# Performance work log

Measured on AMD Instinct MI355X. Metric: run time of the kernel, lower is better.

The kernel has to match this reference:

```python
import jax, jax.numpy as jnp
import numpy as np

PAD = 1
STRIDE = (1, 1)
TEMPERATURE = 1.0


def setup_inputs() -> dict:
    key = jax.random.key(0)
    ks = jax.random.split(key, 5)
    x = jax.random.normal(ks[0], (16, 256, 56, 56), dtype=jnp.float32)
    kernels = jax.random.normal(ks[1], (8, 256, 256, 3, 3), dtype=jnp.float32)
    w1 = jax.random.normal(ks[2], (256, 64), dtype=jnp.float32) * 0.0625
    b1 = jnp.zeros((64,), dtype=jnp.float32)
    w2 = jax.random.normal(ks[3], (64, 8), dtype=jnp.float32) * 0.125
    b2 = jnp.zeros((8,), dtype=jnp.float32)
    return {"x": x, "kernels": kernels, "w1": w1, "b1": b1, "w2": w2, "b2": b2}


def _forward(x, kernels, w1, b1, w2, b2):
    # Attention: global average pool -> MLP -> softmax over kernels
    pooled = jnp.mean(x, axis=(2, 3))                      # [B, C]
    h = jax.nn.relu(pooled @ w1 + b1)                      # [B, H]
    scores = h @ w2 + b2                                   # [B, K]
    alphas = jax.nn.softmax(scores / TEMPERATURE, axis=-1) # [B, K]

    # Per-sample mixed kernels: [B, O, I, kh, kw]
    weighted = jnp.einsum('bk,koihw->boihw', alphas, kernels)

    # Per-sample conv2d (groups=1), vectorized over batch
    def conv_one(xi, wi):
        return jax.lax.conv_general_dilated(
            xi[None], wi, STRIDE, [(PAD, PAD), (PAD, PAD)],
            dimension_numbers=('NCHW', 'OIHW', 'NCHW'))[0]

    return jax.vmap(conv_one)(x, weighted)                 # [B, O, H, W]


def reference(x, kernels, w1, b1, w2, b2):
    return _forward(x, kernels, w1, b1, w2, b2)
```

## Files before the change

### kernel.cpp

```cpp
#include <hip/hip_runtime.h>
#include <hip/hip_bf16.h>
#include <stdint.h>

typedef __attribute__((ext_vector_type(8))) short bf16x8;
typedef __attribute__((ext_vector_type(4))) float f32x4;

#define BATCH 16
#define CH    256
#define HW    56
#define HWHW  3136
#define NK    8

#define XPT_BYTES   30408704ul
#define WK_BYTES    18874368ul
#define POOL_BYTES  16384ul
#define ALPHA_BYTES 512ul

__device__ __forceinline__ void gl_lds16(const void* g, void* l) {
    __builtin_amdgcn_global_load_lds((const __attribute__((address_space(1))) uint32_t*)g,
                                     (__attribute__((address_space(3))) uint32_t*)l, 16, 0, 0);
}

__device__ __forceinline__ float bf16bits_to_f32(short h) {
    return __uint_as_float(((uint32_t)(uint16_t)h) << 16);
}

__global__ void __launch_bounds__(256, 2)
xpose_pool_kernel(const float* __restrict__ x, __hip_bfloat16* __restrict__ xp,
                  float* __restrict__ pooled) {
    __shared__ short tile[2 * 56 * 256];
    const int tid = threadIdx.x;
    const int ys  = blockIdx.x;
    const int b   = blockIdx.y;
    const int y0  = ys * 2;

    const float* xb = x + (size_t)b * CH * HWHW + (size_t)y0 * HW;
    for (int it = 0; it < 28; ++it) {
        int idx = it * 256 + tid;
        int ch  = idx / 28;
        int xi  = idx - ch * 28;
        int r   = xi / 14;
        int x4  = (xi - r * 14) * 4;
        const float4 v = *(const float4*)(xb + (size_t)ch * HWHW + r * HW + x4);
        const float* vf = (const float*)&v;
#pragma unroll
        for (int j = 0; j < 4; ++j) {
            __hip_bfloat16 h = __float2bfloat16(vf[j]);
            tile[(r * 56 + x4 + j) * 256 + (ch ^ (((x4 & 7) | j) << 3))] = *(const short*)&h;
        }
    }
    __syncthreads();

    {
        float s = 0.f;
        const int ch = tid;
        for (int r = 0; r < 2; ++r)
            for (int xx = 0; xx < 56; ++xx)
                s += bf16bits_to_f32(tile[(r * 56 + xx) * 256 + (ch ^ ((xx & 7) << 3))]);
        atomicAdd(&pooled[b * 256 + ch], s * (1.0f / 3136.0f));
    }

    __hip_bfloat16* dst0 = xp + ((size_t)(b * 58 + y0 + 1) * 64 + 1) * 256;
    for (int it = 0; it < 14; ++it) {
        int idx = it * 256 + tid;
        int ch0 = (idx & 31) * 8;
        int pos = idx >> 5;
        int r = pos / 56, xx = pos - (pos / 56) * 56;
        bf16x8 vv = *(const bf16x8*)&tile[(r * 56 + xx) * 256 + (ch0 ^ ((xx & 7) << 3))];
        *(bf16x8*)(dst0 + ((size_t)(r * 64 + xx)) * 256 + ch0) = vv;
    }

    bf16x8 z = {};
    if (tid < 128) {
        int r   = tid >> 6;
        int c2  = (tid >> 5) & 1;
        int ch0 = (tid & 31) * 8;
        *(bf16x8*)(xp + ((size_t)(b * 58 + y0 + 1 + r) * 64 + (c2 ? 57 : 0)) * 256 + ch0) = z;
    }
    if (ys == 0 || ys == 27) {
        int p = (ys == 0) ? 0 : 57;
        __hip_bfloat16* rowp = xp + (size_t)(b * 58 + p) * 64 * 256;
        for (int it = tid; it < 2048; it += 256)
            *(bf16x8*)(rowp + (size_t)it * 8) = z;
    }
}

__global__ void __launch_bounds__(256)
mlp_kernel(const float* __restrict__ pooled,
           const float* __restrict__ w1, const float* __restrict__ b1,
           const float* __restrict__ w2, const float* __restrict__ b2,
           float* __restrict__ alphas) {
    const int b = blockIdx.x;
    __shared__ float pl[256];
    __shared__ float hp[4][64];
    __shared__ float h[64];
    __shared__ float sc[8];
    int t = threadIdx.x;
    pl[t] = pooled[b * 256 + t];
    __syncthreads();
    int j = t & 63, part = t >> 6;
    float s = 0.f;
    const float* w1p = w1 + part * 64 * 64 + j;
#pragma unroll 8
    for (int c = 0; c < 64; ++c) s += pl[part * 64 + c] * w1p[c * 64];
    hp[part][j] = s;
    __syncthreads();
    if (t < 64) h[t] = fmaxf(hp[0][t] + hp[1][t] + hp[2][t] + hp[3][t] + b1[t], 0.f);
    __syncthreads();
    if (t < 8) {
        float acc = b2[t];
#pragma unroll 8
        for (int jj = 0; jj < 64; ++jj) acc += h[jj] * w2[jj * 8 + t];
        sc[t] = acc;
    }
    __syncthreads();
    if (t == 0) {
        float m = sc[0];
#pragma unroll
        for (int k = 1; k < 8; ++k) m = fmaxf(m, sc[k]);
        float ssum = 0.f, e[8];
#pragma unroll
        for (int k = 0; k < 8; ++k) { e[k] = expf(sc[k] - m); ssum += e[k]; }
        float inv = 1.0f / ssum;
#pragma unroll
        for (int k = 0; k < 8; ++k) alphas[b * 8 + k] = e[k] * inv;
    }
}

__global__ void wmix_kernel(const float* __restrict__ kern, const float* __restrict__ alphas,
                            __hip_bfloat16* __restrict__ wk) {
    __shared__ float al[16][8];
    int t = threadIdx.x;
    if (t < 128) al[t >> 3][t & 7] = alphas[t];
    __syncthreads();
    const int o = blockIdx.x, i = t;
    const int idx = o * 256 + i;
    const size_t ibase = (size_t)((i >> 5) * 16384 + ((o >> 4)) * 1024 + (o & 15) * 64 +
                                  ((i >> 3) & 3) * 16 + (i & 7) * 2);
    float kv[8][9];
    const float* kp = kern + (size_t)idx * 9;
#pragma unroll
    for (int k = 0; k < 8; ++k)
#pragma unroll
        for (int q = 0; q < 9; ++q) kv[k][q] = kp[(size_t)k * 589824 + q];
    char* wkb = (char*)wk;
#pragma unroll 1
    for (int b = 0; b < 16; ++b) {
#pragma unroll
        for (int q = 0; q < 9; ++q) {
            float acc = 0.f;
#pragma unroll
            for (int k = 0; k < 8; ++k) acc += al[b][k] * kv[k][q];
            __hip_bfloat16 h = __float2bfloat16(acc);
            *(short*)(wkb + (size_t)(b * 9 + q) * 131072 + ibase) = *(const short*)&h;
        }
    }
}

__global__ void __launch_bounds__(256, 1)
conv_kernel(const __hip_bfloat16* __restrict__ xpT, const __hip_bfloat16* __restrict__ wk,
            float* __restrict__ out) {
    __shared__ short lds_x[2][6 * 64 * 32];

    const int tid   = threadIdx.x;
    const int lane  = tid & 63;
    const int g     = lane >> 4;
    const int l15   = lane & 15;
    const int w     = tid >> 6;
    const int wm    = w >> 1;
    const int wn    = w & 1;
    const int w64   = tid & ~63;

    const int flat  = blockIdx.x;
    const int swzid = (flat & 7) * 56 + (flat >> 3);
    const int b     = swzid / 28;
    const int rem   = swzid - b * 28;
    const int mtile = rem & 1;
    const int y0    = (rem >> 1) * 4;

    int cellb[7], cc[7];
#pragma unroll
    for (int fn = 0; fn < 7; ++fn) {
        int n = wn * 112 + fn * 16 + l15;
        int r = n / 56, c = n % 56;
        cc[fn] = c;
        cellb[fn] = r * 64 + c;
    }

    f32x4 acc[4][7];
#pragma unroll
    for (int fm = 0; fm < 4; ++fm)
#pragma unroll
        for (int fn = 0; fn < 7; ++fn) acc[fm][fn] = (f32x4){0.f, 0.f, 0.f, 0.f};

    const size_t xb = ((size_t)b * 58 + y0) * 64 * 256;
    const char* wkb = (const char*)wk + (size_t)(b * 9) * 131072 +
                      (size_t)((mtile * 8 + wm * 4) * 1024 + l15 * 64 + g * 16);

#define STAGE_X(CI, BUF)                                                            \
    do {                                                                            \
        _Pragma("unroll")                                                           \
        for (int it = 0; it < 6; ++it) {                                            \
            int idx = it * 256 + tid;                                               \
            int sg  = idx & 3, cell = idx >> 2;                                     \
            int c = cell & 63;                                                      \
            int h = sg ^ ((c >> 1) & 3);                                            \
            const __hip_bfloat16* src = xpT + xb + (size_t)cell * 256 + (CI) * 32 + h * 8; \
            gl_lds16(src, (char*)lds_x[BUF] + (it * 256 + w64) * 16);               \
        }                                                                           \
    } while (0)

#define LOADA(KK, AR)                                                               \
    do {                                                                            \
        _Pragma("unroll")                                                           \
        for (int fm = 0; fm < 4; ++fm)                                              \
            AR[fm] = *(const bf16x8*)(wkb + (size_t)((KK) * 131072 + ci * 16384 + fm * 1024)); \
    } while (0)

#define LOADB(KK, BR)                                                               \
    do {                                                                            \
        const int kh = (KK) / 3, kw = (KK) % 3;                                     \
        _Pragma("unroll")                                                           \
        for (int fn = 0; fn < 7; ++fn) {                                            \
            int cell = cellb[fn] + kh * 64 + kw;                                    \
            int slot = g ^ (((cc[fn] + kw) >> 1) & 3);                              \
            BR[fn] = *(const bf16x8*)(xlds + cell * 64 + (slot << 4));              \
        }                                                                           \
    } while (0)

#define MM(AR, BR)                                                                  \
    do {                                                                            \
        __builtin_amdgcn_s_setprio(1);                                              \
        _Pragma("unroll")                                                           \
        for (int fn = 0; fn < 7; ++fn)                                              \
            _Pragma("unroll")                                                       \
            for (int fm = 0; fm < 4; ++fm)                                          \
                acc[fm][fn] = __builtin_amdgcn_mfma_f32_16x16x32_bf16(AR[fm], BR[fn], acc[fm][fn], 0, 0, 0); \
        __builtin_amdgcn_s_setprio(0);                                              \
    } while (0)

    STAGE_X(0, 0);
    __syncthreads();

#pragma unroll 1
    for (int ci = 0; ci < 8; ++ci) {
        const char* xlds = (const char*)lds_x[ci & 1];
        bf16x8 afA[4], afB[4], bfA[7], bfB[7];
        LOADA(0, afA); LOADB(0, bfA);
        if (ci < 7) STAGE_X(ci + 1, (ci & 1) ^ 1);
        LOADA(1, afB); LOADB(1, bfB);
        MM(afA, bfA);
        LOADA(2, afA); LOADB(2, bfA); MM(afB, bfB);
        LOADA(3, afB); LOADB(3, bfB); MM(afA, bfA);
        LOADA(4, afA); LOADB(4, bfA); MM(afB, bfB);
        LOADA(5, afB); LOADB(5, bfB); MM(afA, bfA);
        LOADA(6, afA); LOADB(6, bfA); MM(afB, bfB);
        LOADA(7, afB); LOADB(7, bfB); MM(afA, bfA);
        LOADA(8, afA); LOADB(8, bfA); MM(afB, bfB);
        MM(afA, bfA);
        if (ci < 7) __syncthreads();
    }

    const int mbase = mtile * 128 + wm * 64;
#pragma unroll
    for (int fm = 0; fm < 4; ++fm)
#pragma unroll
        for (int fn = 0; fn < 7; ++fn) {
            int n = wn * 112 + fn * 16 + l15;
            int r = n / 56, c = n - (n / 56) * 56;
            int o = mbase + fm * 16 + 4 * g;
            float* op = out + (((size_t)b * 256 + o) * 56 + (y0 + r)) * 56 + c;
#pragma unroll
            for (int q = 0; q < 4; ++q) op[(size_t)q * HWHW] = acc[fm][fn][q];
        }
#undef STAGE_X
#undef LOADA
#undef LOADB
#undef MM
}

extern "C" void kernel_launch(void* const* d_in, const int* in_sizes, int n_in,
                              void* d_out, int out_size, void* d_ws, size_t ws_size,
                              hipStream_t stream) {
    const float* x    = (const float*)d_in[0];
    const float* kern = (const float*)d_in[1];
    const float* w1   = (const float*)d_in[2];
    const float* b1   = (const float*)d_in[3];
    const float* w2   = (const float*)d_in[4];
    const float* b2   = (const float*)d_in[5];
    float* out = (float*)d_out;

    char* wsp = (char*)d_ws;
    __hip_bfloat16* xpT    = (__hip_bfloat16*)wsp;
    __hip_bfloat16* wkbuf  = (__hip_bfloat16*)(wsp + XPT_BYTES);
    float*          pooled = (float*)(wsp + XPT_BYTES + WK_BYTES);
    float*          alphas = (float*)(wsp + XPT_BYTES + WK_BYTES + POOL_BYTES);

    hipMemsetAsync(pooled, 0, POOL_BYTES, stream);

    xpose_pool_kernel<<<dim3(28, 16), dim3(256), 0, stream>>>(x, xpT, pooled);
    mlp_kernel<<<dim3(16), dim3(256), 0, stream>>>(pooled, w1, b1, w2, b2, alphas);
    wmix_kernel<<<dim3(256), dim3(256), 0, stream>>>(kern, alphas, wkbuf);
    conv_kernel<<<dim3(448), dim3(256), 0, stream>>>(xpT, wkbuf, out);
}
```

Before: 236.8 us.

## Split conv work across eight waves with smaller per-wave tiles and change transpose swizzle

The conv kernel moves to 512 threads per block, with each wave computing a 32x112 output tile instead of 64x112. This halves accumulator registers and raises launch-bound occupancy. B fragments are now loaded right before their MFMAs rather than double-buffered in registers. The transpose kernel's LDS swizzle changes to XOR on the 4-wide column group. In exchange, each block reads more LDS for B fragments and loses explicit register prefetch of B.

```diff
diff --git a/kernel.cpp b/kernel.cpp
--- a/kernel.cpp
+++ b/kernel.cpp
@@ -43,10 +43,11 @@
         int x4  = (xi - r * 14) * 4;
         const float4 v = *(const float4*)(xb + (size_t)ch * HWHW + r * HW + x4);
         const float* vf = (const float*)&v;
+        int xr = ch ^ (((x4 >> 2) & 7) << 3);
 #pragma unroll
         for (int j = 0; j < 4; ++j) {
             __hip_bfloat16 h = __float2bfloat16(vf[j]);
-            tile[(r * 56 + x4 + j) * 256 + (ch ^ (((x4 & 7) | j) << 3))] = *(const short*)&h;
+            tile[(r * 56 + x4 + j) * 256 + xr] = *(const short*)&h;
         }
     }
     __syncthreads();
@@ -56,7 +57,7 @@
         const int ch = tid;
         for (int r = 0; r < 2; ++r)
             for (int xx = 0; xx < 56; ++xx)
-                s += bf16bits_to_f32(tile[(r * 56 + xx) * 256 + (ch ^ ((xx & 7) << 3))]);
+                s += bf16bits_to_f32(tile[(r * 56 + xx) * 256 + (ch ^ (((xx >> 2) & 7) << 3))]);
         atomicAdd(&pooled[b * 256 + ch], s * (1.0f / 3136.0f));
     }
 
@@ -66,7 +67,7 @@
         int ch0 = (idx & 31) * 8;
         int pos = idx >> 5;
         int r = pos / 56, xx = pos - (pos / 56) * 56;
-        bf16x8 vv = *(const bf16x8*)&tile[(r * 56 + xx) * 256 + (ch0 ^ ((xx & 7) << 3))];
+        bf16x8 vv = *(const bf16x8*)&tile[(r * 56 + xx) * 256 + (ch0 ^ (((xx >> 2) & 7) << 3))];
         *(bf16x8*)(dst0 + ((size_t)(r * 64 + xx)) * 256 + ch0) = vv;
     }
 
@@ -157,7 +158,7 @@
     }
 }
 
-__global__ void __launch_bounds__(256, 1)
+__global__ void __launch_bounds__(512, 4)
 conv_kernel(const __hip_bfloat16* __restrict__ xpT, const __hip_bfloat16* __restrict__ wk,
             float* __restrict__ out) {
     __shared__ short lds_x[2][6 * 64 * 32];
@@ -178,64 +179,59 @@
     const int mtile = rem & 1;
     const int y0    = (rem >> 1) * 4;
 
-    int cellb[7], cc[7];
+    int cellb[7];
 #pragma unroll
     for (int fn = 0; fn < 7; ++fn) {
         int n = wn * 112 + fn * 16 + l15;
-        int r = n / 56, c = n % 56;
-        cc[fn] = c;
-        cellb[fn] = r * 64 + c;
-    }
-
-    f32x4 acc[4][7];
-#pragma unroll
-    for (int fm = 0; fm < 4; ++fm)
+        cellb[fn] = (n / 56) * 64 + (n % 56);
+    }
+
+    f32x4 acc[2][7];
+#pragma unroll
+    for (int fm = 0; fm < 2; ++fm)
 #pragma unroll
         for (int fn = 0; fn < 7; ++fn) acc[fm][fn] = (f32x4){0.f, 0.f, 0.f, 0.f};
 
     const size_t xb = ((size_t)b * 58 + y0) * 64 * 256;
     const char* wkb = (const char*)wk + (size_t)(b * 9) * 131072 +
-                      (size_t)((mtile * 8 + wm * 4) * 1024 + l15 * 64 + g * 16);
+                      (size_t)((mtile * 8 + wm * 2) * 1024 + l15 * 64 + g * 16);
 
 #define STAGE_X(CI, BUF)                                                            \
     do {                                                                            \
         _Pragma("unroll")                                                           \
-        for (int it = 0; it < 6; ++it) {                                            \
-            int idx = it * 256 + tid;                                               \
+        for (int it = 0; it < 3; ++it) {                                            \
+            int idx = it * 512 + tid;                                               \
             int sg  = idx & 3, cell = idx >> 2;                                     \
             int c = cell & 63;                                                      \
             int h = sg ^ ((c >> 1) & 3);                                            \
             const __hip_bfloat16* src = xpT + xb + (size_t)cell * 256 + (CI) * 32 + h * 8; \
-            gl_lds16(src, (char*)lds_x[BUF] + (it * 256 + w64) * 16);               \
+            gl_lds16(src, (char*)lds_x[BUF] + (it * 512 + w64) * 16);               \
         }                                                                           \
     } while (0)
 
 #define LOADA(KK, AR)                                                               \
     do {                                                                            \
         _Pragma("unroll")                                                           \
-        for (int fm = 0; fm < 4; ++fm)                                              \
+        for (int fm = 0; fm < 2; ++fm)                                              \
             AR[fm] = *(const bf16x8*)(wkb + (size_t)((KK) * 131072 + ci * 16384 + fm * 1024)); \
     } while (0)
 
-#define LOADB(KK, BR)                                                               \
+#define STEPB(KK, AR)                                                               \
     do {                                                                            \
         const int kh = (KK) / 3, kw = (KK) % 3;                                     \
+        bf16x8 bf[7];                                                               \
         _Pragma("unroll")                                                           \
         for (int fn = 0; fn < 7; ++fn) {                                            \
             int cell = cellb[fn] + kh * 64 + kw;                                    \
-            int slot = g ^ (((cc[fn] + kw) >> 1) & 3);                              \
-            BR[fn] = *(const bf16x8*)(xlds + cell * 64 + (slot << 4));              \
+            int slot = g ^ ((((cellb[fn] & 63) + kw) >> 1) & 3);                    \
+            bf[fn] = *(const bf16x8*)(xlds + cell * 64 + (slot << 4));              \
         }                                                                           \
-    } while (0)
-
-#define MM(AR, BR)                                                                  \
-    do {                                                                            \
         __builtin_amdgcn_s_setprio(1);                                              \
         _Pragma("unroll")                                                           \
         for (int fn = 0; fn < 7; ++fn)                                              \
             _Pragma("unroll")                                                       \
-            for (int fm = 0; fm < 4; ++fm)                                          \
-                acc[fm][fn] = __builtin_amdgcn_mfma_f32_16x16x32_bf16(AR[fm], BR[fn], acc[fm][fn], 0, 0, 0); \
+            for (int fm = 0; fm < 2; ++fm)                                          \
+                acc[fm][fn] = __builtin_amdgcn_mfma_f32_16x16x32_bf16(AR[fm], bf[fn], acc[fm][fn], 0, 0, 0); \
         __builtin_amdgcn_s_setprio(0);                                              \
     } while (0)
 
@@ -245,25 +241,25 @@
 #pragma unroll 1
     for (int ci = 0; ci < 8; ++ci) {
         const char* xlds = (const char*)lds_x[ci & 1];
-        bf16x8 afA[4], afB[4], bfA[7], bfB[7];
-        LOADA(0, afA); LOADB(0, bfA);
+        bf16x8 afA[2], afB[2];
+        LOADA(0, afA);
         if (ci < 7) STAGE_X(ci + 1, (ci & 1) ^ 1);
-        LOADA(1, afB); LOADB(1, bfB);
-        MM(afA, bfA);
-        LOADA(2, afA); LOADB(2, bfA); MM(afB, bfB);
-        LOADA(3, afB); LOADB(3, bfB); MM(afA, bfA);
-        LOADA(4, afA); LOADB(4, bfA); MM(afB, bfB);
-        LOADA(5, afB); LOADB(5, bfB); MM(afA, bfA);
-        LOADA(6, afA); LOADB(6, bfA); MM(afB, bfB);
-        LOADA(7, afB); LOADB(7, bfB); MM(afA, bfA);
-        LOADA(8, afA); LOADB(8, bfA); MM(afB, bfB);
-        MM(afA, bfA);
+        LOADA(1, afB);
+        STEPB(0, afA); LOADA(2, afA);
+        STEPB(1, afB); LOADA(3, afB);
+        STEPB(2, afA); LOADA(4, afA);
+        STEPB(3, afB); LOADA(5, afB);
+        STEPB(4, afA); LOADA(6, afA);
+        STEPB(5, afB); LOADA(7, afB);
+        STEPB(6, afA); LOADA(8, afA);
+        STEPB(7, afB);
+        STEPB(8, afA);
         if (ci < 7) __syncthreads();
     }
 
-    const int mbase = mtile * 128 + wm * 64;
-#pragma unroll
-    for (int fm = 0; fm < 4; ++fm)
+    const int mbase = mtile * 128 + wm * 32;
+#pragma unroll
+    for (int fm = 0; fm < 2; ++fm)
 #pragma unroll
         for (int fn = 0; fn < 7; ++fn) {
             int n = wn * 112 + fn * 16 + l15;
@@ -275,8 +271,7 @@
         }
 #undef STAGE_X
 #undef LOADA
-#undef LOADB
-#undef MM
+#undef STEPB
 }
 
 extern "C" void kernel_launch(void* const* d_in, const int* in_sizes, int n_in,
@@ -301,5 +296,5 @@
     xpose_pool_kernel<<<dim3(28, 16), dim3(256), 0, stream>>>(x, xpT, pooled);
     mlp_kernel<<<dim3(16), dim3(256), 0, stream>>>(pooled, w1, b1, w2, b2, alphas);
     wmix_kernel<<<dim3(256), dim3(256), 0, stream>>>(kern, alphas, wkbuf);
-    conv_kernel<<<dim3(448), dim3(256), 0, stream>>>(xpT, wkbuf, out);
-}
+    conv_kernel<<<dim3(448), dim3(512), 0, stream>>>(xpT, wkbuf, out);
+}
```

Result: slower. 288.6 us (+21.9%).
